# Kernel tuning notes

Hardware: AMD Instinct MI355X
Metric: run time of the kernel (lower is better)

Reference implementation:

```python
import jax, jax.numpy as jnp
import numpy as np


def conv2d(x, w, pad=0, groups=1, bias=None):
    out = jax.lax.conv_general_dilated(
        x, w, (1, 1), [(pad, pad), (pad, pad)],
        dimension_numbers=('NCHW', 'OIHW', 'NCHW'), feature_group_count=groups)
    return out if bias is None else out + bias[None, :, None, None]


def l2norm(t):
    # F.normalize(t, dim=-1): divide by max(||t||_2, 1e-12)
    return t / jnp.maximum(jnp.sqrt(jnp.sum(t * t, axis=-1, keepdims=True)), 1e-12)


def chan_attn(q, k, v, temp, heads):
    # transposed (channel) attention: contract over N=H*W, softmax over small channel dim
    b, _, h, w = v.shape
    n = h * w
    q = l2norm(q.reshape(b, heads, -1, n))
    k = l2norm(k.reshape(b, heads, -1, n))
    v = v.reshape(b, heads, -1, n)
    attn = jax.nn.softmax(jnp.einsum('bhdn,bhen->bhde', q, k) * temp, axis=-1)
    return jnp.einsum('bhde,bhen->bhdn', attn, v).reshape(b, -1, h, w)


def nearest_resize(x, H, W):
    # torch F.interpolate(mode='nearest'): idx = floor(i * in/out)
    hi, wi = x.shape[2], x.shape[3]
    iy = jnp.arange(H) * hi // H
    ix = jnp.arange(W) * wi // W
    return x[:, :, iy][:, :, :, ix]


def deform_conv(x, offsets, w, bias, k, pad, groups):
    # torchvision DeformConv2d, stride=1, dilation=1, offset layout [B, 2*k*k, H, W] as (dy, dx) pairs
    B, Cin, H, W = x.shape
    K2 = k * k
    off = offsets.reshape(B, K2, 2, H, W)
    ky, kx = jnp.meshgrid(jnp.arange(k), jnp.arange(k), indexing='ij')
    py = (jnp.arange(H)[None, None, :, None] - pad) + ky.reshape(1, K2, 1, 1) + off[:, :, 0]
    px = (jnp.arange(W)[None, None, None, :] - pad) + kx.reshape(1, K2, 1, 1) + off[:, :, 1]
    y0f = jnp.floor(py); x0f = jnp.floor(px)
    wy = (py - y0f)[:, None]  # [B,1,K2,H,W]
    wx = (px - x0f)[:, None]
    y0 = y0f.astype(jnp.int32); x0 = x0f.astype(jnp.int32)
    xf = x.reshape(B, Cin, H * W)

    def gather(yi, xi):
        valid = ((yi >= 0) & (yi < H) & (xi >= 0) & (xi < W)).astype(x.dtype)
        idx = (jnp.clip(yi, 0, H - 1) * W + jnp.clip(xi, 0, W - 1)).reshape(B, 1, -1)
        v = jnp.take_along_axis(xf, idx, axis=2).reshape(B, Cin, K2, H, W)
        return v * valid[:, None]

    s = (gather(y0, x0) * (1 - wy) * (1 - wx)
         + gather(y0, x0 + 1) * (1 - wy) * wx
         + gather(y0 + 1, x0) * wy * (1 - wx)
         + gather(y0 + 1, x0 + 1) * wy * wx)  # [B, Cin, K2, H, W]
    g = groups
    s = s.reshape(B, g, Cin // g, K2, H, W)
    wg = w.reshape(g, w.shape[0] // g, Cin // g, K2)
    out = jnp.einsum('bgckhw,gock->bgohw', s, wg).reshape(B, -1, H, W)
    return out + bias[None, :, None, None]


def scconv(x, w_k2, w_k3, w_k4):
    B, C, H, W = x.shape
    p = x.reshape(B, C, H // 2, 2, W // 2, 2).mean(axis=(3, 5))  # AvgPool2d(2,2)
    a = jax.nn.sigmoid(nearest_resize(conv2d(p, w_k2, pad=0), H, W))
    return conv2d(conv2d(x, w_k3, pad=1) * a, w_k4, pad=1)


def layernorm_c(x, g, b):
    # LayerNorm over channel dim of NCHW (applied as [B, HW, C] in the original)
    b_, c, h, w = x.shape
    t = x.reshape(b_, c, h * w).transpose(0, 2, 1)
    mu = t.mean(-1, keepdims=True)
    var = ((t - mu) ** 2).mean(-1, keepdims=True)
    t = (t - mu) / jnp.sqrt(var + 1e-5) * g + b
    return t.transpose(0, 2, 1).reshape(b_, c, h, w)


def _forward(x, y, temp, w_po, w_lp1, w_lp2, ln_g, ln_b, temp_in, w_qkv, w_qkvd,
             w_mproj, w_c3, w_k2, w_k3, w_k4, w_d3, b_d3, w_d5, b_d5, w_d7, b_d7,
             w_pw, b_pw):
    b, c, h, w = x.shape
    heads = 8
    # --- Multi_Receptive_Attentive_Prompts ---
    l1 = conv2d(x, w_lp1)
    l2 = conv2d(x, w_lp2, pad=1)
    xn = layernorm_c(x, ln_g, ln_b)
    qkv = conv2d(conv2d(xn, w_qkv), w_qkvd, pad=1, groups=c)
    qi, ki, vi = jnp.split(qkv, 3, axis=1)
    xg = x + conv2d(chan_attn(qi, ki, vi, temp_in, heads), w_mproj)
    prompt = conv2d(jnp.concatenate([l1, l2, xg], axis=1), w_c3, pad=1)
    # --- Temporal_Alignment ---
    offs = scconv(jnp.concatenate([x, y], axis=1), w_k2, w_k3, w_k4)  # [B,166,H,W]
    f3 = jax.nn.relu(deform_conv(x, offs[:, :18], w_d3, b_d3, 3, 1, 8))
    f5 = jax.nn.relu(deform_conv(x, offs[:, 18:68], w_d5, b_d5, 5, 2, 8))
    f7 = jax.nn.relu(deform_conv(x, offs[:, 68:166], w_d7, b_d7, 7, 3, 8))
    k_feat = conv2d(jnp.concatenate([f3, f5, f7], axis=1), w_pw, bias=b_pw)
    # --- prompted channel attention ---
    q_feat = jnp.concatenate([x, prompt], axis=1)  # 2c channels -> d_q = 2c/heads
    out = chan_attn(q_feat, k_feat, x, temp, heads)  # [B, 2c, H, W]
    return conv2d(out, w_po)


def setup_inputs() -> dict:
    key = jax.random.key(0)
    ks = jax.random.split(key, 16)
    C, B, H, W = 32, 2, 128, 128
    r = lambda k, shp: jax.random.normal(k, shp, dtype=jnp.float32) * 0.05
    return {
        'x': jax.random.normal(ks[0], (B, C, H, W), dtype=jnp.float32),
        'y': jax.random.normal(ks[1], (B, C, H, W), dtype=jnp.float32),
        'temp': jnp.ones((1, 8, 1, 1), jnp.float32),
        'w_po': r(ks[2], (C, 2 * C, 1, 1)),
        'w_lp1': r(ks[3], (C, C, 1, 1)),
        'w_lp2': r(ks[4], (C, C, 3, 3)),
        'ln_g': jnp.ones((C,), jnp.float32),
        'ln_b': jnp.zeros((C,), jnp.float32),
        'temp_in': jnp.ones((1, 8, 1, 1), jnp.float32),
        'w_qkv': r(ks[5], (3 * C, C, 1, 1)),
        'w_qkvd': r(ks[6], (3 * C, 3, 3, 3)),  # groups=C: in/groups = 3
        'w_mproj': r(ks[7], (C, C, 1, 1)),
        'w_c3': r(ks[8], (C, 3 * C, 3, 3)),
        'w_k2': r(ks[9], (166, 2 * C, 3, 3)),
        'w_k3': r(ks[10], (166, 2 * C, 3, 3)),
        'w_k4': r(ks[11], (166, 166, 3, 3)),
        'w_d3': r(ks[12], (C, C // 8, 3, 3)),
        'b_d3': jnp.zeros((C,), jnp.float32),
        'w_d5': r(ks[13], (C, C // 8, 5, 5)),
        'b_d5': jnp.zeros((C,), jnp.float32),
        'w_d7': r(ks[14], (C, C // 8, 7, 7)),
        'b_d7': jnp.zeros((C,), jnp.float32),
        'w_pw': r(ks[15], (C, 3 * C, 1, 1)),
        'b_pw': jnp.zeros((C,), jnp.float32),
    }


def reference(x, y, temp, w_po, w_lp1, w_lp2, ln_g, ln_b, temp_in, w_qkv, w_qkvd,
              w_mproj, w_c3, w_k2, w_k3, w_k4, w_d3, b_d3, w_d5, b_d5, w_d7, b_d7,
              w_pw, b_pw):
    return _forward(x, y, temp, w_po, w_lp1, w_lp2, ln_g, ln_b, temp_in, w_qkv,
                    w_qkvd, w_mproj, w_c3, w_k2, w_k3, w_k4, w_d3, b_d3, w_d5,
                    b_d5, w_d7, b_d7, w_pw, b_pw)
```

## Files before the change

kernel.cpp:

```cpp
#include <hip/hip_runtime.h>
#include <hip/hip_bf16.h>
#include <hip/hip_fp16.h>


constexpr int B = 2, C = 32, H = 128, W = 128, N = H * W;

using bh8   = __attribute__((ext_vector_type(8))) short;
using f32x4 = __attribute__((ext_vector_type(4))) float;

__device__ __forceinline__ ushort f2bf(float v) {
  __hip_bfloat16 h = __float2bfloat16(v);
  return *(ushort*)&h;
}
__device__ __forceinline__ float bf2f(ushort u) {
  union { unsigned int i; float f; } w; w.i = ((unsigned int)u) << 16; return w.f;
}

__global__ __launch_bounds__(256) void k_prep(const float* __restrict__ x,
                                              const float* __restrict__ y,
                                              const float* __restrict__ ln_g,
                                              const float* __restrict__ ln_b,
                                              float* __restrict__ cat2,
                                              ushort* __restrict__ xtb,
                                              ushort* __restrict__ cat2b,
                                              float* __restrict__ xn) {
  __shared__ float tile[C][257];
  const int b = blockIdx.y, n0 = blockIdx.x * 256, tid = threadIdx.x;
  const int n = n0 + tid;
  for (int c = 0; c < C; c++) {
    float v = x[(size_t)(b * C + c) * N + n];
    tile[c][tid] = v;
    cat2[(size_t)(b * 64 + c) * N + n] = v;
  }
  __syncthreads();
  {
    float s = 0.f, ss = 0.f;
#pragma unroll
    for (int c = 0; c < C; c++) { const float v = tile[c][tid]; s += v; ss += v * v; }
    const float mu = s * (1.f / C);
    const float var = ss * (1.f / C) - mu * mu;
    const float inv = rsqrtf(var + 1e-5f);
#pragma unroll
    for (int c = 0; c < C; c++)
      xn[(size_t)(b * C + c) * N + n] = (tile[c][tid] - mu) * inv * ln_g[c] + ln_b[c];
  }
  for (int i = tid; i < C * 256; i += 256) {
    int c = i & 31, nl = i >> 5;
    const ushort bv = f2bf(tile[c][nl]);
    xtb[((size_t)b * N + n0 + nl) * 32 + c] = bv;
    cat2b[((size_t)b * N + n0 + nl) * 64 + c] = bv;
  }
  __syncthreads();
  for (int c = 0; c < C; c++) {
    float v = y[(size_t)(b * C + c) * N + n];
    tile[c][tid] = v;
    cat2[(size_t)(b * 64 + 32 + c) * N + n] = v;
  }
  __syncthreads();
  for (int i = tid; i < C * 256; i += 256) {
    int c = i & 31, nl = i >> 5;
    cat2b[((size_t)b * N + n0 + nl) * 64 + 32 + c] = f2bf(tile[c][nl]);
  }
}

struct WEnt { const float* src; ushort* dst; int cout_real, cin_real, kc32, total; };
struct WArgs { WEnt e[5]; };

__global__ __launch_bounds__(256) void k_wpack(WArgs a) {
  const WEnt en = a.e[blockIdx.y];
  const int tk = 9 * en.kc32;
  for (int i = blockIdx.x * 256 + threadIdx.x; i < en.total; i += gridDim.x * 256) {
    const int co = i / tk, rem = i - co * tk;
    const int t = rem / en.kc32, ci = rem - t * en.kc32;
    float v = 0.f;
    if (co < en.cout_real && ci < en.cin_real)
      v = en.src[((size_t)co * en.cin_real + ci) * 9 + t];
    en.dst[i] = f2bf(v);
  }
}

__global__ __launch_bounds__(256)
void k_conv3m(const ushort* __restrict__ xin, long in_bs, int in_cs, int ih, int iw,
              const ushort* __restrict__ wp, int kchunks, int cout_real,
              void* __restrict__ outp, long out_bs, int out_coff,
              int oh, int ow, int pad, int omode, int out_cs, int store_tot) {
  __shared__ ushort smem[17408];
  ushort* xt = smem;
  const int tid = threadIdx.x, b = blockIdx.z;
  const int y0 = blockIdx.x * 2, co0 = blockIdx.y * 64;
  const int wv = tid >> 6, lane = tid & 63;
  const int row_sel = wv >> 1, col0 = (wv & 1) * 64;
  const int q = lane >> 4, n = lane & 15, q8 = q * 8;
  const int kc32 = kchunks * 32;
  const ushort* xb = xin + (size_t)b * in_bs;

  f32x4 acc[4][4];
#pragma unroll
  for (int mt = 0; mt < 4; mt++)
#pragma unroll
    for (int nb = 0; nb < 4; nb++) acc[mt][nb] = (f32x4){0.f, 0.f, 0.f, 0.f};

  for (int cc = 0; cc < kchunks; cc++) {
    __syncthreads();
    for (int i = tid; i < 2080; i += 256) {
      const int qq = i & 3, rc = i >> 2;
      const int r = rc / 130, c = rc - r * 130;
      const int yy = y0 - pad + r, xx = c - pad;
      bh8 v = {0, 0, 0, 0, 0, 0, 0, 0};
      if (yy >= 0 && yy < ih && xx >= 0 && xx < iw)
        v = *(const bh8*)(xb + ((size_t)yy * iw + xx) * in_cs + cc * 32 + qq * 8);
      *(bh8*)&xt[rc * 32 + qq * 8] = v;
    }
    __syncthreads();
#pragma unroll
    for (int t = 0; t < 9; t++) {
      const int dy = t / 3, dx = t - dy * 3;
      bh8 a[4], bb[4];
#pragma unroll
      for (int mt = 0; mt < 4; mt++)
        a[mt] = *(const bh8*)(wp + (size_t)((co0 + mt * 16 + n) * 9 + t) * kc32 + cc * 32 + q8);
#pragma unroll
      for (int nb = 0; nb < 4; nb++)
        bb[nb] = *(const bh8*)&xt[((row_sel + dy) * 130 + col0 + nb * 16 + n + dx) * 32 + q8];
#pragma unroll
      for (int mt = 0; mt < 4; mt++)
#pragma unroll
        for (int nb = 0; nb < 4; nb++)
          acc[mt][nb] = __builtin_amdgcn_mfma_f32_16x16x32_bf16(a[mt], bb[nb], acc[mt][nb], 0, 0, 0);
    }
  }

  const size_t osp = (size_t)oh * ow;
  if (omode == 0) {
    const int oy = y0 + row_sel;
    float* ob = (float*)outp + (size_t)b * out_bs + (size_t)out_coff * osp + (size_t)oy * ow;
#pragma unroll
    for (int mt = 0; mt < 4; mt++)
#pragma unroll
      for (int r = 0; r < 4; r++) {
        const int co = co0 + mt * 16 + q * 4 + r;
        if (co < cout_real) {
#pragma unroll
          for (int nb = 0; nb < 4; nb++) {
            const int px = col0 + nb * 16 + n;
            if (px < ow) ob[(size_t)co * osp + px] = acc[mt][nb][r];
          }
        }
      }
  } else if (omode == 1) {
    __syncthreads();
#pragma unroll
    for (int mt = 0; mt < 4; mt++)
#pragma unroll
      for (int nb = 0; nb < 4; nb++) {
        const int px = col0 + nb * 16 + n;
        ushort4 o;
        o.x = f2bf(acc[mt][nb][0]); o.y = f2bf(acc[mt][nb][1]);
        o.z = f2bf(acc[mt][nb][2]); o.w = f2bf(acc[mt][nb][3]);
        *(ushort4*)&smem[(row_sel * 128 + px) * 68 + mt * 16 + q * 4] = o;
      }
    __syncthreads();
    {
      const int row = tid >> 7, px = tid & 127;
      const int oy2 = y0 + row;
      const int sc = min(64, store_tot - co0);
      if (px < ow && sc > 0) {
        ushort* dst = (ushort*)outp + ((size_t)b * osp + (size_t)oy2 * ow + px) * out_cs
                      + out_coff + co0;
        const ushort* src = &smem[(row * 128 + px) * 68];
        for (int c = 0; c < sc; c += 4)
          *(ushort4*)(dst + c) = *(const ushort4*)(src + c);
      }
    }
  } else {
    float* tf = (float*)smem;
    for (int round = 0; round < 2; round++) {
      __syncthreads();
      if (row_sel == round) {
#pragma unroll
        for (int mt = 0; mt < 4; mt++)
#pragma unroll
          for (int nb = 0; nb < 4; nb++) {
            const int px = col0 + nb * 16 + n;
            *(f32x4*)&tf[px * 66 + mt * 16 + q * 4] = acc[mt][nb];
          }
      }
      __syncthreads();
      const int px = tid & 127, ch = tid >> 7;
      const int oy2 = y0 + round;
      float* dst = (float*)outp + ((size_t)b * osp + (size_t)oy2 * ow + px) * out_cs
                   + out_coff + co0 + ch * 32;
      const float* src = &tf[px * 66 + ch * 32];
      for (int c = 0; c < 32; c += 4) {
        if (co0 + ch * 32 + c + 3 < store_tot)
          *(float4*)(dst + c) = *(const float4*)(src + c);
      }
    }
  }
}

template <int PX>
__global__ __launch_bounds__(256)
void k_conv1x1v(const float* __restrict__ in, long in_bs, int cin,
                const float* __restrict__ wts, const float* __restrict__ bias,
                float* __restrict__ out, long out_bs, int out_coff,
                ushort* __restrict__ outb, int ob_cs) {
  const int n0 = (blockIdx.x * 256 + threadIdx.x) * PX;
  const int co0 = blockIdx.y * 4, b = blockIdx.z;
  const float* ip = in + (size_t)b * in_bs + n0;
  const float* w = wts + (size_t)co0 * cin;
  float acc[4][PX] = {};
  for (int ci = 0; ci < cin; ci++) {
    float xv[PX];
    if (PX == 4) {
      const float4 v = *(const float4*)(ip + (size_t)ci * N);
      xv[0] = v.x; xv[1] = v.y; xv[2] = v.z; xv[3] = v.w;
    } else {
      const float2 v = *(const float2*)(ip + (size_t)ci * N);
      xv[0] = v.x; xv[1] = v.y;
    }
    const float w0 = w[ci], w1 = w[cin + ci], w2 = w[2 * cin + ci], w3 = w[3 * cin + ci];
#pragma unroll
    for (int p = 0; p < PX; p++) {
      acc[0][p] += xv[p] * w0; acc[1][p] += xv[p] * w1;
      acc[2][p] += xv[p] * w2; acc[3][p] += xv[p] * w3;
    }
  }
  if (bias) {
#pragma unroll
    for (int o = 0; o < 4; o++) {
      const float bv = bias[co0 + o];
#pragma unroll
      for (int p = 0; p < PX; p++) acc[o][p] += bv;
    }
  }
  if (outb) {
#pragma unroll
    for (int p = 0; p < PX; p++) {
      ushort4 o;
      o.x = f2bf(acc[0][p]); o.y = f2bf(acc[1][p]);
      o.z = f2bf(acc[2][p]); o.w = f2bf(acc[3][p]);
      *(ushort4*)(outb + ((size_t)b * N + n0 + p) * ob_cs + out_coff + co0) = o;
    }
  } else {
#pragma unroll
    for (int o = 0; o < 4; o++) {
      if (PX == 4)
        *(float4*)(out + (size_t)b * out_bs + (size_t)(out_coff + co0 + o) * N + n0) =
            make_float4(acc[o][0], acc[o][1], acc[o][2], acc[o][3]);
      else
        *(float2*)(out + (size_t)b * out_bs + (size_t)(out_coff + co0 + o) * N + n0) =
            make_float2(acc[o][0], acc[o][1]);
    }
  }
}

__global__ __launch_bounds__(256) void k_dwconv(const float* __restrict__ in,
                                                const float* __restrict__ wts,
                                                float* __restrict__ out) {
  const int n0 = (blockIdx.x * 256 + threadIdx.x) * 4;
  const int g = blockIdx.y, b = blockIdx.z;
  const int h0 = n0 >> 7, w0 = n0 & 127;
  float acc[3][4] = {};
  for (int ci = 0; ci < 3; ci++) {
    const float* ip = in + ((size_t)b * 96 + g * 3 + ci) * N;
    float v[3][6];
#pragma unroll
    for (int r = 0; r < 3; r++) {
      const int iy = h0 - 1 + r;
      const bool rowok = (iy >= 0) & (iy < H);
#pragma unroll
      for (int j = 0; j < 6; j++) {
        const int ix = w0 - 1 + j;
        v[r][j] = (rowok && ix >= 0 && ix < W) ? ip[(size_t)iy * W + ix] : 0.f;
      }
    }
#pragma unroll
    for (int o = 0; o < 3; o++) {
      const float* wp = wts + ((size_t)(g * 3 + o) * 3 + ci) * 9;
#pragma unroll
      for (int r = 0; r < 3; r++) {
        const float wa = wp[r * 3 + 0], wb = wp[r * 3 + 1], wc = wp[r * 3 + 2];
#pragma unroll
        for (int p = 0; p < 4; p++)
          acc[o][p] += v[r][p] * wa + v[r][p + 1] * wb + v[r][p + 2] * wc;
      }
    }
  }
#pragma unroll
  for (int o = 0; o < 3; o++)
    *(float4*)(out + ((size_t)b * 96 + g * 3 + o) * N + n0) =
        make_float4(acc[o][0], acc[o][1], acc[o][2], acc[o][3]);
}

template <int DQ>
__global__ __launch_bounds__(256)
void k_attn_part(const float* __restrict__ q1, long q1_bs,
                 const float* __restrict__ q2, long q2_bs,
                 const float* __restrict__ k, long k_bs,
                 float* __restrict__ partial) {
  const int h = blockIdx.x, b = blockIdx.y, ch = blockIdx.z, tid = threadIdx.x;
  const float* qp[DQ];
#pragma unroll
  for (int d = 0; d < DQ; d++) {
    const int qc = h * DQ + d;
    qp[d] = (qc < 32) ? (q1 + (size_t)b * q1_bs + (size_t)qc * N)
                      : (q2 + (size_t)b * q2_bs + (size_t)(qc - 32) * N);
  }
  const float* kp[4];
#pragma unroll
  for (int e = 0; e < 4; e++) kp[e] = k + (size_t)b * k_bs + (size_t)(h * 4 + e) * N;

  constexpr int NV = DQ + 4 + DQ * 4;
  float ssq[DQ] = {}, ssk[4] = {}, gr[DQ][4] = {};
  const int n1 = (ch + 1) * (N / 8);
  for (int n = ch * (N / 8) + tid; n < n1; n += 256) {
    float qv[DQ], kv[4];
#pragma unroll
    for (int d = 0; d < DQ; d++) { qv[d] = qp[d][n]; ssq[d] += qv[d] * qv[d]; }
#pragma unroll
    for (int e = 0; e < 4; e++) { kv[e] = kp[e][n]; ssk[e] += kv[e] * kv[e]; }
#pragma unroll
    for (int d = 0; d < DQ; d++)
#pragma unroll
      for (int e = 0; e < 4; e++) gr[d][e] += qv[d] * kv[e];
  }
  float vals[NV];
#pragma unroll
  for (int d = 0; d < DQ; d++) vals[d] = ssq[d];
#pragma unroll
  for (int e = 0; e < 4; e++) vals[DQ + e] = ssk[e];
#pragma unroll
  for (int d = 0; d < DQ; d++)
#pragma unroll
    for (int e = 0; e < 4; e++) vals[DQ + 4 + d * 4 + e] = gr[d][e];
#pragma unroll
  for (int j = 0; j < NV; j++) {
    float v = vals[j];
    for (int m = 32; m > 0; m >>= 1) v += __shfl_xor(v, m, 64);
    vals[j] = v;
  }
  __shared__ float red[4][NV];
  const int wid = tid >> 6, lane = tid & 63;
  if (lane == 0)
#pragma unroll
    for (int j = 0; j < NV; j++) red[wid][j] = vals[j];
  __syncthreads();
  if (tid < NV)
    partial[(size_t)(((b * 8 + h) * 8) + ch) * NV + tid] =
        red[0][tid] + red[1][tid] + red[2][tid] + red[3][tid];
}

template <int DQ>
__global__ __launch_bounds__(128)
void k_attn_soft(const float* __restrict__ partial,
                 const float* __restrict__ temp, float* __restrict__ stats) {
  constexpr int NV = DQ + 4 + DQ * 4;
  const int h = blockIdx.x, b = blockIdx.y, tid = threadIdx.x;
  __shared__ float tot[NV];
  if (tid < NV) {
    float s = 0.f;
#pragma unroll
    for (int ch = 0; ch < 8; ch++)
      s += partial[(size_t)(((b * 8 + h) * 8) + ch) * NV + tid];
    tot[tid] = s;
  }
  __syncthreads();
  if (tid == 0) {
    float invq[DQ], invk[4];
#pragma unroll
    for (int d = 0; d < DQ; d++) invq[d] = 1.f / fmaxf(sqrtf(tot[d]), 1e-12f);
#pragma unroll
    for (int e = 0; e < 4; e++) invk[e] = 1.f / fmaxf(sqrtf(tot[DQ + e]), 1e-12f);
    const float t = temp[h];
    float* sp = stats + (size_t)(b * 8 + h) * DQ * 4;
    for (int d = 0; d < DQ; d++) {
      float s[4], mx = -1e30f;
#pragma unroll
      for (int e = 0; e < 4; e++) {
        s[e] = tot[DQ + 4 + d * 4 + e] * invq[d] * invk[e] * t;
        mx = fmaxf(mx, s[e]);
      }
      float sum = 0.f;
#pragma unroll
      for (int e = 0; e < 4; e++) { s[e] = expf(s[e] - mx); sum += s[e]; }
#pragma unroll
      for (int e = 0; e < 4; e++) sp[d * 4 + e] = s[e] / sum;
    }
  }
}

template <int DQ>
__global__ __launch_bounds__(256)
void k_fold(const float* __restrict__ stats, const float* __restrict__ w,
            float* __restrict__ M) {
  const int b = blockIdx.x;
  for (int idx = threadIdx.x; idx < 1024; idx += 256) {
    const int co = idx >> 5, j = idx & 31;
    const int h = j >> 2, e = j & 3;
    const float* A = stats + ((size_t)b * 8 + h) * DQ * 4;
    const float* wr = w + co * (8 * DQ) + h * DQ;
    float s = 0.f;
#pragma unroll
    for (int d = 0; d < DQ; d++) s += wr[d] * A[d * 4 + e];
    M[((size_t)b * 32 + co) * 32 + j] = s;
  }
}

__global__ __launch_bounds__(256)
void k_attn_mproj2(const float* __restrict__ qkv2, const float* __restrict__ M2,
                   const float* __restrict__ x, ushort* __restrict__ cat1b) {
  __shared__ float mls[512];
  const int tid = threadIdx.x, b = blockIdx.y, z = blockIdx.z;
  const int n = blockIdx.x * 256 + tid;
  for (int i = tid; i < 512; i += 256)
    mls[i] = M2[((size_t)b * 32 + z * 16) * 32 + i];
  __syncthreads();
  const float* vi = qkv2 + (size_t)b * (96L * N) + 64L * N;
  float vv[32];
#pragma unroll
  for (int ci = 0; ci < 32; ci++) vv[ci] = vi[(size_t)ci * N + n];
  ushort to[16];
  for (int o = 0; o < 16; o++) {
    const float* m = &mls[o * 32];
    float r = 0.f;
#pragma unroll
    for (int ci = 0; ci < 32; ci += 4) {
      const float4 w4 = *(const float4*)&m[ci];
      r += w4.x * vv[ci] + w4.y * vv[ci + 1] + w4.z * vv[ci + 2] + w4.w * vv[ci + 3];
    }
    r += x[(size_t)(b * 64 + z * 16 + o) * N + n];
    to[o] = f2bf(r);
  }
  ushort* dp = cat1b + ((size_t)b * N + n) * 96 + 64 + z * 16;
#pragma unroll
  for (int k = 0; k < 2; k++) *(bh8*)(dp + k * 8) = *(const bh8*)&to[k * 8];
}

__global__ __launch_bounds__(256)
void k_attn_po2(const float* __restrict__ cat2, const float* __restrict__ M,
                float* __restrict__ outp) {
  __shared__ float mls[512];
  const int tid = threadIdx.x, b = blockIdx.y, z = blockIdx.z;
  const int n = blockIdx.x * 256 + tid;
  for (int i = tid; i < 512; i += 256)
    mls[i] = M[((size_t)b * 32 + z * 16) * 32 + i];
  __syncthreads();
  const float* v = cat2 + (size_t)b * (64L * N);
  float vv[32];
#pragma unroll
  for (int ci = 0; ci < 32; ci++) vv[ci] = v[(size_t)ci * N + n];
  for (int o = 0; o < 16; o++) {
    const float* m = &mls[o * 32];
    float r = 0.f;
#pragma unroll
    for (int ci = 0; ci < 32; ci += 4) {
      const float4 w4 = *(const float4*)&m[ci];
      r += w4.x * vv[ci] + w4.y * vv[ci + 1] + w4.z * vv[ci + 2] + w4.w * vv[ci + 3];
    }
    outp[(size_t)(b * 32 + z * 16 + o) * N + n] = r;
  }
}

__global__ __launch_bounds__(256) void k_avgpoolb(const float* __restrict__ in,
                                                  ushort* __restrict__ outb) {
  const int opx = blockIdx.x * 256 + threadIdx.x;
  const int b = blockIdx.y;
  const int ox = opx & 63, oy = opx >> 6;
  const float* p0 = in + (size_t)b * 64 * N + (size_t)(oy * 2) * W + ox * 2;
  ushort tmp[64];
#pragma unroll
  for (int c = 0; c < 64; c++) {
    const float* p = p0 + (size_t)c * N;
    tmp[c] = f2bf(0.25f * (p[0] + p[1] + p[W] + p[W + 1]));
  }
  ushort* dp = outb + ((size_t)b * 4096 + opx) * 64;
#pragma unroll
  for (int k = 0; k < 8; k++) *(bh8*)(dp + k * 8) = *(const bh8*)&tmp[k * 8];
}

__global__ __launch_bounds__(256)
void k_sigcast(const ushort* __restrict__ t3r, const float* __restrict__ asmall,
               ushort* __restrict__ t3b) {
  const int n = blockIdx.x * 256 + threadIdx.x;
  const int cy = blockIdx.y, b = blockIdx.z;
  const int x = n & 127, yv = n >> 7;
  const int iy = (yv * 62) >> 7, ix = (x * 62) >> 7;
  const ushort* sp = t3r + ((size_t)b * N + n) * 192 + cy * 32;
  ushort tr[32];
#pragma unroll
  for (int k = 0; k < 4; k++) *(bh8*)&tr[k * 8] = *(const bh8*)(sp + k * 8);
  ushort tmp[32];
#pragma unroll
  for (int j = 0; j < 32; j++) {
    const int c = cy * 32 + j;
    float v = 0.f;
    if (c < 166) {
      const float a = asmall[((size_t)b * 166 + c) * 3844 + iy * 62 + ix];
      v = bf2f(tr[j]) * (1.f / (1.f + expf(-a)));
    }
    tmp[j] = f2bf(v);
  }
  ushort* dp = t3b + ((size_t)b * N + n) * 192 + cy * 32;
#pragma unroll
  for (int k = 0; k < 4; k++) *(bh8*)(dp + k * 8) = *(const bh8*)&tmp[k * 8];
}

__global__ __launch_bounds__(256)
void k_deform7(const ushort* __restrict__ xtb, const float* __restrict__ offs,
               const float* __restrict__ wd3, const float* __restrict__ bd3,
               const float* __restrict__ wd5, const float* __restrict__ bd5,
               const float* __restrict__ wd7, const float* __restrict__ bd7,
               float* __restrict__ out) {
  const int tid = threadIdx.x, b = blockIdx.y;
  const int zone = blockIdx.x >> 9;
  const int blk = blockIdx.x & 511;
  int K, off_c0, out_c0;
  const float *wd, *bd;
  if (zone == 0)      { K = 3; off_c0 = 0;  out_c0 = 0;  wd = wd3; bd = bd3; }
  else if (zone == 1) { K = 5; off_c0 = 18; out_c0 = 32; wd = wd5; bd = bd5; }
  else                { K = 7; off_c0 = 68; out_c0 = 64; wd = wd7; bd = bd7; }
  const int K2 = K * K, PAD = K / 2;

  extern __shared__ __align__(16) char smem[];
  __half*  wlds = (__half*)smem;
  __half*  wbl  = wlds + K2 * 128;
  ushort*  abl  = (ushort*)(wbl + 32 * K2 * 4);

  for (int i = tid; i < K2 * 128; i += 256) {
    const int t = i >> 7, r = i & 127;
    const int g = r >> 4, oo = (r >> 2) & 3, ci = r & 3;
    wlds[i] = __float2half(wd[(size_t)((g * 4 + oo) * 4 + ci) * K2 + t]);
  }
  const int px0 = blk * 32;
  const float* obb = offs + ((size_t)b * N) * 168;
  for (int i = tid; i < 32 * K2; i += 256) {
    const int p = i / K2, t = i - p * K2;
    const int px = px0 + p;
    const int hy = px >> 7, wx = px & 127;
    const int ky = t / K, kx = t - ky * K;
    const float* ob2 = obb + (size_t)px * 168 + off_c0;
    const float dy = ob2[2 * t];
    const float dx = ob2[2 * t + 1];
    const float py = (float)(hy - PAD + ky) + dy;
    const float pxf = (float)(wx - PAD + kx) + dx;
    const float y0f = floorf(py), x0f = floorf(pxf);
    const float fy = py - y0f, fx = pxf - x0f;
    const int y0 = (int)y0f, x0 = (int)x0f;
    const int y1 = y0 + 1, x1 = x0 + 1;
    float w00 = (1.f - fy) * (1.f - fx), w01 = (1.f - fy) * fx;
    float w10 = fy * (1.f - fx), w11 = fy * fx;
    const bool vy0 = (y0 >= 0) & (y0 < H), vy1 = (y1 >= 0) & (y1 < H);
    const bool vx0 = (x0 >= 0) & (x0 < W), vx1 = (x1 >= 0) & (x1 < W);
    w00 = (vy0 & vx0) ? w00 : 0.f;
    w01 = (vy0 & vx1) ? w01 : 0.f;
    w10 = (vy1 & vx0) ? w10 : 0.f;
    w11 = (vy1 & vx1) ? w11 : 0.f;
    const int cy0 = min(max(y0, 0), H - 1), cy1 = min(max(y1, 0), H - 1);
    const int cx0 = min(max(x0, 0), W - 1), cx1 = min(max(x1, 0), W - 1);
    const int base = (p * K2 + t) * 4;
    wbl[base + 0] = __float2half(w00); wbl[base + 1] = __float2half(w01);
    wbl[base + 2] = __float2half(w10); wbl[base + 3] = __float2half(w11);
    abl[base + 0] = (ushort)(cy0 * W + cx0);
    abl[base + 1] = (ushort)(cy0 * W + cx1);
    abl[base + 2] = (ushort)(cy1 * W + cx0);
    abl[base + 3] = (ushort)(cy1 * W + cx1);
  }
  __syncthreads();

  const int pxl = tid >> 3, g = tid & 7;
  const int px = px0 + pxl;
  const ushort* xb = xtb + (size_t)b * N * 32 + g * 4;
  float acc[4] = {0.f, 0.f, 0.f, 0.f};
  for (int t = 0; t < K2; t++) {
    const int base = (pxl * K2 + t) * 4;
    const ushort4 r4 = *(const ushort4*)&abl[base];
    const float2 w01v = __half22float2(*(const __half2*)&wbl[base]);
    const float2 w23v = __half22float2(*(const __half2*)&wbl[base + 2]);
    const ushort4 c0 = *(const ushort4*)(xb + (size_t)r4.x * 32);
    const ushort4 c1 = *(const ushort4*)(xb + (size_t)r4.y * 32);
    const ushort4 c2 = *(const ushort4*)(xb + (size_t)r4.z * 32);
    const ushort4 c3 = *(const ushort4*)(xb + (size_t)r4.w * 32);
    const float s0 = w01v.x * bf2f(c0.x) + w01v.y * bf2f(c1.x)
                   + w23v.x * bf2f(c2.x) + w23v.y * bf2f(c3.x);
    const float s1 = w01v.x * bf2f(c0.y) + w01v.y * bf2f(c1.y)
                   + w23v.x * bf2f(c2.y) + w23v.y * bf2f(c3.y);
    const float s2 = w01v.x * bf2f(c0.z) + w01v.y * bf2f(c1.z)
                   + w23v.x * bf2f(c2.z) + w23v.y * bf2f(c3.z);
    const float s3 = w01v.x * bf2f(c0.w) + w01v.y * bf2f(c1.w)
                   + w23v.x * bf2f(c2.w) + w23v.y * bf2f(c3.w);
    const __half2* wp2 = (const __half2*)&wlds[(t * 8 + g) * 16];
#pragma unroll
    for (int oo = 0; oo < 4; oo++) {
      const float2 u01 = __half22float2(wp2[oo * 2]);
      const float2 u23 = __half22float2(wp2[oo * 2 + 1]);
      acc[oo] += s0 * u01.x + s1 * u01.y + s2 * u23.x + s3 * u23.y;
    }
  }
#pragma unroll
  for (int oo = 0; oo < 4; oo++) {
    const float r = fmaxf(acc[oo] + bd[g * 4 + oo], 0.f);
    out[((size_t)b * 96 + out_c0 + g * 4 + oo) * N + px] = r;
  }
}

extern "C" void kernel_launch(void* const* d_in, const int* in_sizes, int n_in,
                              void* d_out, int out_size, void* d_ws, size_t ws_size,
                              hipStream_t stream) {
  const float* fx       = (const float*)d_in[0];
  const float* fy       = (const float*)d_in[1];
  const float* w_temp   = (const float*)d_in[2];
  const float* w_po     = (const float*)d_in[3];
  const float* w_lp1    = (const float*)d_in[4];
  const float* w_lp2    = (const float*)d_in[5];
  const float* ln_g     = (const float*)d_in[6];
  const float* ln_b     = (const float*)d_in[7];
  const float* w_tempin = (const float*)d_in[8];
  const float* w_qkv    = (const float*)d_in[9];
  const float* w_qkvd   = (const float*)d_in[10];
  const float* w_mproj  = (const float*)d_in[11];
  const float* w_c3     = (const float*)d_in[12];
  const float* w_k2     = (const float*)d_in[13];
  const float* w_k3     = (const float*)d_in[14];
  const float* w_k4     = (const float*)d_in[15];
  const float* w_d3     = (const float*)d_in[16];
  const float* b_d3     = (const float*)d_in[17];
  const float* w_d5     = (const float*)d_in[18];
  const float* b_d5     = (const float*)d_in[19];
  const float* w_d7     = (const float*)d_in[20];
  const float* b_d7     = (const float*)d_in[21];
  const float* w_pw     = (const float*)d_in[22];
  const float* b_pw     = (const float*)d_in[23];
  float* ws = (float*)d_ws;

  size_t off = 0;
  auto buf = [&](size_t nelem) { float* p = ws + off; off += nelem; return p; };
  float* CAT2   = buf(2097152);
  float* XTBf   = buf(1048576);
  float* R1     = buf(1048576);
  float* R2     = buf(3145728);
  float* R3     = buf(3145728);
  float* PROMPT = buf(1048576);
  float* R4     = buf(5439488);
  float* OFFS   = buf(5505024);
  float* STATS  = buf(32768);
  float* CAT2Bf = buf(524288);
  float* WPf    = buf(327680);
  (void)ws_size; (void)out_size; (void)n_in; (void)in_sizes;

  float* XN = R1;
  float* QKV1 = R2;
  float* QKV2 = R3;   float* ASMALL = R3 + 524288;
  float* CAT3 = R4;   float* KFEAT = R4 + 3145728;
  float* ST_IN = STATS;
  float* ST_FI = STATS + 256;
  float* P_IN  = STATS + 1024;
  float* P_FI  = STATS + 8192;
  float* M_IN  = STATS + 16384;
  float* M_FI  = STATS + 20480;

  ushort* XTb   = (ushort*)XTBf;
  ushort* CAT2b = (ushort*)CAT2Bf;
  ushort* POOLb = (ushort*)R3;
  ushort* CAT1b = (ushort*)OFFS;
  ushort* T3raw = (ushort*)R4;
  ushort* T3b   = (ushort*)R2;

  ushort* WPu = (ushort*)WPf;
  ushort* wp_lp2 = WPu;
  ushort* wp_c3  = wp_lp2 + 18432;
  ushort* wp_k2  = wp_c3 + 55296;
  ushort* wp_k3  = wp_k2 + 110592;
  ushort* wp_k4  = wp_k3 + 110592;

  const long bs64 = 64L * N, bs32 = 32L * N, bs96 = 96L * N;

  WArgs wa;
  wa.e[0] = { w_lp2, wp_lp2, 32, 32, 32, 64 * 9 * 32 };
  wa.e[1] = { w_c3,  wp_c3,  32, 96, 96, 64 * 9 * 96 };
  wa.e[2] = { w_k2,  wp_k2, 166, 64, 64, 192 * 9 * 64 };
  wa.e[3] = { w_k3,  wp_k3, 166, 64, 64, 192 * 9 * 64 };
  wa.e[4] = { w_k4,  wp_k4, 166, 166, 192, 192 * 9 * 192 };
  k_wpack<<<dim3(64, 5), 256, 0, stream>>>(wa);
  k_prep<<<dim3(N / 256, B), 256, 0, stream>>>(fx, fy, ln_g, ln_b, CAT2, XTb, CAT2b, XN);
  k_conv1x1v<4><<<dim3(N / 1024, 24, B), 256, 0, stream>>>(
      XN, bs32, 32, w_qkv, nullptr, QKV1, bs96, 0, nullptr, 0);
  k_dwconv<<<dim3(N / 1024, 32, B), 256, 0, stream>>>(QKV1, w_qkvd, QKV2);
  k_attn_part<4><<<dim3(8, B, 8), 256, 0, stream>>>(
      QKV2, bs96, nullptr, 0, QKV2 + bs32, bs96, P_IN);
  k_attn_soft<4><<<dim3(8, B), 128, 0, stream>>>(P_IN, w_tempin, ST_IN);
  k_fold<4><<<dim3(B), 256, 0, stream>>>(ST_IN, w_mproj, M_IN);
  k_attn_mproj2<<<dim3(N / 256, B, 2), 256, 0, stream>>>(QKV2, M_IN, CAT2, CAT1b);
  k_conv1x1v<2><<<dim3(N / 512, 8, B), 256, 0, stream>>>(
      CAT2, bs64, 32, w_lp1, nullptr, nullptr, 0, 0, CAT1b, 96);
  k_conv3m<<<dim3(64, 1, B), 256, 0, stream>>>(
      CAT2b, (long)N * 64, 64, H, W, wp_lp2, 1, 32, CAT1b, 0, 32, H, W, 1, 1, 96, 32);
  k_conv3m<<<dim3(64, 1, B), 256, 0, stream>>>(
      CAT1b, (long)N * 96, 96, H, W, wp_c3, 3, 32, PROMPT, bs32, 0, H, W, 1, 0, 0, 0);
  k_avgpoolb<<<dim3(16, B), 256, 0, stream>>>(CAT2, POOLb);
  k_conv3m<<<dim3(31, 3, B), 256, 0, stream>>>(
      POOLb, 4096L * 64, 64, 64, 64, wp_k2, 2, 166, ASMALL, 166L * 3844, 0, 62, 62, 0, 0, 0, 0);
  k_conv3m<<<dim3(64, 3, B), 256, 0, stream>>>(
      CAT2b, (long)N * 64, 64, H, W, wp_k3, 2, 166, T3raw, 0, 0, H, W, 1, 1, 192, 192);
  k_sigcast<<<dim3(64, 6, B), 256, 0, stream>>>(T3raw, ASMALL, T3b);
  k_conv3m<<<dim3(64, 3, B), 256, 0, stream>>>(
      T3b, (long)N * 192, 192, H, W, wp_k4, 6, 166, OFFS, 0, 0, H, W, 1, 2, 168, 168);
  {
    const int K2m = 49;
    const size_t smem = (size_t)K2m * 128 * 2 + (size_t)32 * K2m * 4 * 2 * 2;
    k_deform7<<<dim3(3 * (N / 32), B), 256, smem, stream>>>(
        XTb, OFFS, w_d3, b_d3, w_d5, b_d5, w_d7, b_d7, CAT3);
  }
  k_conv1x1v<2><<<dim3(N / 512, 8, B), 256, 0, stream>>>(
      CAT3, bs96, 96, w_pw, b_pw, KFEAT, bs32, 0, nullptr, 0);
  k_attn_part<8><<<dim3(8, B, 8), 256, 0, stream>>>(
      CAT2, bs64, PROMPT, bs32, KFEAT, bs32, P_FI);
  k_attn_soft<8><<<dim3(8, B), 128, 0, stream>>>(P_FI, w_temp, ST_FI);
  k_fold<8><<<dim3(B), 256, 0, stream>>>(ST_FI, w_po, M_FI);
  k_attn_po2<<<dim3(N / 256, B, 2), 256, 0, stream>>>(CAT2, M_FI, (float*)d_out);
}
```

Measured before the change: 492.0 us.

## Fuse avgpool into prep kernel and split deform taps across thread halves

The 2x2 average pool that feeds the downsampled conv is now computed inside the prep kernel from its shared-memory tile, which removes a separate kernel launch and a second read of CAT2. The pooled result gets its own buffer. The deformable conv kernel now handles 16 pixels per block instead of 32, doubling the grid. Two thread halves each take alternate kernel taps and combine their partial sums through shared memory, which adds parallelism at the cost of an extra barrier and reduction.

```diff
diff --git a/kernel.cpp b/kernel.cpp
--- a/kernel.cpp
+++ b/kernel.cpp
@@ -23,10 +23,12 @@
                                               float* __restrict__ cat2,
                                               ushort* __restrict__ xtb,
                                               ushort* __restrict__ cat2b,
-                                              float* __restrict__ xn) {
+                                              float* __restrict__ xn,
+                                              ushort* __restrict__ poolb) {
   __shared__ float tile[C][257];
   const int b = blockIdx.y, n0 = blockIdx.x * 256, tid = threadIdx.x;
   const int n = n0 + tid;
+  const int prow = blockIdx.x;
   for (int c = 0; c < C; c++) {
     float v = x[(size_t)(b * C + c) * N + n];
     tile[c][tid] = v;
@@ -50,6 +52,12 @@
     xtb[((size_t)b * N + n0 + nl) * 32 + c] = bv;
     cat2b[((size_t)b * N + n0 + nl) * 64 + c] = bv;
   }
+  for (int i = tid; i < 2048; i += 256) {
+    const int ox = i >> 5, c = i & 31;
+    const float pv = 0.25f * (tile[c][2 * ox] + tile[c][2 * ox + 1]
+                            + tile[c][128 + 2 * ox] + tile[c][128 + 2 * ox + 1]);
+    poolb[((size_t)b * 4096 + prow * 64 + ox) * 64 + c] = f2bf(pv);
+  }
   __syncthreads();
   for (int c = 0; c < C; c++) {
     float v = y[(size_t)(b * C + c) * N + n];
@@ -60,6 +68,12 @@
   for (int i = tid; i < C * 256; i += 256) {
     int c = i & 31, nl = i >> 5;
     cat2b[((size_t)b * N + n0 + nl) * 64 + 32 + c] = f2bf(tile[c][nl]);
+  }
+  for (int i = tid; i < 2048; i += 256) {
+    const int ox = i >> 5, c = i & 31;
+    const float pv = 0.25f * (tile[c][2 * ox] + tile[c][2 * ox + 1]
+                            + tile[c][128 + 2 * ox] + tile[c][128 + 2 * ox + 1]);
+    poolb[((size_t)b * 4096 + prow * 64 + ox) * 64 + 32 + c] = f2bf(pv);
   }
 }
 
@@ -462,23 +476,6 @@
   }
 }
 
-__global__ __launch_bounds__(256) void k_avgpoolb(const float* __restrict__ in,
-                                                  ushort* __restrict__ outb) {
-  const int opx = blockIdx.x * 256 + threadIdx.x;
-  const int b = blockIdx.y;
-  const int ox = opx & 63, oy = opx >> 6;
-  const float* p0 = in + (size_t)b * 64 * N + (size_t)(oy * 2) * W + ox * 2;
-  ushort tmp[64];
-#pragma unroll
-  for (int c = 0; c < 64; c++) {
-    const float* p = p0 + (size_t)c * N;
-    tmp[c] = f2bf(0.25f * (p[0] + p[1] + p[W] + p[W + 1]));
-  }
-  ushort* dp = outb + ((size_t)b * 4096 + opx) * 64;
-#pragma unroll
-  for (int k = 0; k < 8; k++) *(bh8*)(dp + k * 8) = *(const bh8*)&tmp[k * 8];
-}
-
 __global__ __launch_bounds__(256)
 void k_sigcast(const ushort* __restrict__ t3r, const float* __restrict__ asmall,
                ushort* __restrict__ t3b) {
@@ -507,14 +504,14 @@
 }
 
 __global__ __launch_bounds__(256)
-void k_deform7(const ushort* __restrict__ xtb, const float* __restrict__ offs,
+void k_deform8(const ushort* __restrict__ xtb, const float* __restrict__ offs,
                const float* __restrict__ wd3, const float* __restrict__ bd3,
                const float* __restrict__ wd5, const float* __restrict__ bd5,
                const float* __restrict__ wd7, const float* __restrict__ bd7,
                float* __restrict__ out) {
   const int tid = threadIdx.x, b = blockIdx.y;
-  const int zone = blockIdx.x >> 9;
-  const int blk = blockIdx.x & 511;
+  const int zone = blockIdx.x >> 10;
+  const int blk = blockIdx.x & 1023;
   int K, off_c0, out_c0;
   const float *wd, *bd;
   if (zone == 0)      { K = 3; off_c0 = 0;  out_c0 = 0;  wd = wd3; bd = bd3; }
@@ -525,16 +522,17 @@
   extern __shared__ __align__(16) char smem[];
   __half*  wlds = (__half*)smem;
   __half*  wbl  = wlds + K2 * 128;
-  ushort*  abl  = (ushort*)(wbl + 32 * K2 * 4);
+  ushort*  abl  = (ushort*)(wbl + 16 * K2 * 4);
+  float*   pbuf = (float*)(abl + 16 * K2 * 4);
 
   for (int i = tid; i < K2 * 128; i += 256) {
     const int t = i >> 7, r = i & 127;
     const int g = r >> 4, oo = (r >> 2) & 3, ci = r & 3;
     wlds[i] = __float2half(wd[(size_t)((g * 4 + oo) * 4 + ci) * K2 + t]);
   }
-  const int px0 = blk * 32;
+  const int px0 = blk * 16;
   const float* obb = offs + ((size_t)b * N) * 168;
-  for (int i = tid; i < 32 * K2; i += 256) {
+  for (int i = tid; i < 16 * K2; i += 256) {
     const int p = i / K2, t = i - p * K2;
     const int px = px0 + p;
     const int hy = px >> 7, wx = px & 127;
@@ -568,11 +566,10 @@
   }
   __syncthreads();
 
-  const int pxl = tid >> 3, g = tid & 7;
-  const int px = px0 + pxl;
+  const int pxl = tid >> 4, half = (tid >> 3) & 1, g = tid & 7;
   const ushort* xb = xtb + (size_t)b * N * 32 + g * 4;
   float acc[4] = {0.f, 0.f, 0.f, 0.f};
-  for (int t = 0; t < K2; t++) {
+  for (int t = half; t < K2; t += 2) {
     const int base = (pxl * K2 + t) * 4;
     const ushort4 r4 = *(const ushort4*)&abl[base];
     const float2 w01v = __half22float2(*(const __half2*)&wbl[base]);
@@ -597,10 +594,17 @@
       acc[oo] += s0 * u01.x + s1 * u01.y + s2 * u23.x + s3 * u23.y;
     }
   }
-#pragma unroll
-  for (int oo = 0; oo < 4; oo++) {
-    const float r = fmaxf(acc[oo] + bd[g * 4 + oo], 0.f);
-    out[((size_t)b * 96 + out_c0 + g * 4 + oo) * N + px] = r;
+  if (half == 1)
+    *(f32x4*)&pbuf[(pxl * 8 + g) * 4] = *(f32x4*)acc;
+  __syncthreads();
+  if (half == 0) {
+    const f32x4 p4 = *(const f32x4*)&pbuf[(pxl * 8 + g) * 4];
+    const int px = px0 + pxl;
+#pragma unroll
+    for (int oo = 0; oo < 4; oo++) {
+      const float r = fmaxf(acc[oo] + p4[oo] + bd[g * 4 + oo], 0.f);
+      out[((size_t)b * 96 + out_c0 + g * 4 + oo) * N + px] = r;
+    }
   }
 }
 
@@ -646,6 +650,7 @@
   float* STATS  = buf(32768);
   float* CAT2Bf = buf(524288);
   float* WPf    = buf(327680);
+  float* POOLBf = buf(262144);
   (void)ws_size; (void)out_size; (void)n_in; (void)in_sizes;
 
   float* XN = R1;
@@ -661,7 +666,7 @@
 
   ushort* XTb   = (ushort*)XTBf;
   ushort* CAT2b = (ushort*)CAT2Bf;
-  ushort* POOLb = (ushort*)R3;
+  ushort* POOLb = (ushort*)POOLBf;
   ushort* CAT1b = (ushort*)OFFS;
   ushort* T3raw = (ushort*)R4;
   ushort* T3b   = (ushort*)R2;
@@ -682,7 +687,8 @@
   wa.e[3] = { w_k3,  wp_k3, 166, 64, 64, 192 * 9 * 64 };
   wa.e[4] = { w_k4,  wp_k4, 166, 166, 192, 192 * 9 * 192 };
   k_wpack<<<dim3(64, 5), 256, 0, stream>>>(wa);
-  k_prep<<<dim3(N / 256, B), 256, 0, stream>>>(fx, fy, ln_g, ln_b, CAT2, XTb, CAT2b, XN);
+  k_prep<<<dim3(N / 256, B), 256, 0, stream>>>(
+      fx, fy, ln_g, ln_b, CAT2, XTb, CAT2b, XN, POOLb);
   k_conv1x1v<4><<<dim3(N / 1024, 24, B), 256, 0, stream>>>(
       XN, bs32, 32, w_qkv, nullptr, QKV1, bs96, 0, nullptr, 0);
   k_dwconv<<<dim3(N / 1024, 32, B), 256, 0, stream>>>(QKV1, w_qkvd, QKV2);
@@ -697,7 +703,6 @@
       CAT2b, (long)N * 64, 64, H, W, wp_lp2, 1, 32, CAT1b, 0, 32, H, W, 1, 1, 96, 32);
   k_conv3m<<<dim3(64, 1, B), 256, 0, stream>>>(
       CAT1b, (long)N * 96, 96, H, W, wp_c3, 3, 32, PROMPT, bs32, 0, H, W, 1, 0, 0, 0);
-  k_avgpoolb<<<dim3(16, B), 256, 0, stream>>>(CAT2, POOLb);
   k_conv3m<<<dim3(31, 3, B), 256, 0, stream>>>(
       POOLb, 4096L * 64, 64, 64, 64, wp_k2, 2, 166, ASMALL, 166L * 3844, 0, 62, 62, 0, 0, 0, 0);
   k_conv3m<<<dim3(64, 3, B), 256, 0, stream>>>(
@@ -707,8 +712,10 @@
       T3b, (long)N * 192, 192, H, W, wp_k4, 6, 166, OFFS, 0, 0, H, W, 1, 2, 168, 168);
   {
     const int K2m = 49;
-    const size_t smem = (size_t)K2m * 128 * 2 + (size_t)32 * K2m * 4 * 2 * 2;
-    k_deform7<<<dim3(3 * (N / 32), B), 256, smem, stream>>>(
+    const size_t smem = (size_t)K2m * 128 * 2
+                      + (size_t)16 * K2m * 4 * 2 * 2
+                      + (size_t)16 * 8 * 4 * 4;
+    k_deform8<<<dim3(3 * (N / 16), B), 256, smem, stream>>>(
         XTb, OFFS, w_d3, b_d3, w_d5, b_d5, w_d7, b_d7, CAT3);
   }
   k_conv1x1v<2><<<dim3(N / 512, 8, B), 256, 0, stream>>>(
```

After: 497.8 us. No clear change (+1.2%).
